# Kernel optimization log

Measured on AMD Instinct MI355X. Metric: run time of the kernel, lower is better.

Reference implementation:

```python
import jax, jax.numpy as jnp
import numpy as np
from jax import lax

IN_H, IN_W = 328, 512
ANCHOR_W, ANCHOR_H = 0.2, 0.29
CONF_T, IOU_T, K_DET = 0.2, 0.3, 10
EPS = 1e-5


def setup_inputs() -> dict:
    key = jax.random.key(0)
    ks = jax.random.split(key, 20)
    f = jnp.float32
    d = {}
    d['features'] = jax.random.normal(ks[0], (16, 512, 4, 21, 32), f)
    d['conv1_w'] = jax.random.normal(ks[1], (256, 512, 3, 3, 3), f) * np.float32(np.sqrt(2.0 / (512 * 27)))
    d['conv1_b'] = jnp.zeros((256,), f)
    d['bn1_g'] = 1.0 + 0.1 * jax.random.normal(ks[2], (256,), f)
    d['bn1_b'] = 0.1 * jax.random.normal(ks[3], (256,), f)
    d['bn1_m'] = 0.1 * jax.random.normal(ks[4], (256,), f)
    d['bn1_v'] = 0.5 + jax.random.uniform(ks[5], (256,), f)
    d['conv2_w'] = jax.random.normal(ks[6], (128, 256, 3, 3, 3), f) * np.float32(np.sqrt(2.0 / (256 * 27)))
    d['conv2_b'] = jnp.zeros((128,), f)
    d['bn2_g'] = 1.0 + 0.1 * jax.random.normal(ks[7], (128,), f)
    d['bn2_b'] = 0.1 * jax.random.normal(ks[8], (128,), f)
    d['bn2_m'] = 0.1 * jax.random.normal(ks[9], (128,), f)
    d['bn2_v'] = 0.5 + jax.random.uniform(ks[10], (128,), f)
    d['conv3_w'] = jax.random.normal(ks[11], (8, 128, 1, 1, 1), f) * np.float32(np.sqrt(2.0 / 128))
    d['conv3_b'] = jnp.zeros((8,), f)
    d['cls_w'] = 0.01 * jax.random.normal(ks[12], (2, 512), f)
    d['cls_b'] = jnp.zeros((2,), f)
    d['sev_w'] = 0.01 * jax.random.normal(ks[13], (4, 512), f)
    d['sev_b'] = jnp.zeros((4,), f)
    return d


def conv3d(x, w, b, pad):
    y = lax.conv_general_dilated(x, w, (1, 1, 1), [(pad, pad)] * 3,
                                 dimension_numbers=('NCDHW', 'OIDHW', 'NCDHW'))
    return y + b[None, :, None, None, None]


def bn3d(x, g, b, m, v):
    inv = g * lax.rsqrt(v + EPS)
    return x * inv[None, :, None, None, None] + (b - m * inv)[None, :, None, None, None]


def _iou_one_vs_all(box, boxes):
    x1 = jnp.maximum(box[0], boxes[:, 0]); y1 = jnp.maximum(box[1], boxes[:, 1])
    x2 = jnp.minimum(box[2], boxes[:, 2]); y2 = jnp.minimum(box[3], boxes[:, 3])
    inter = jnp.clip(x2 - x1, 0.0) * jnp.clip(y2 - y1, 0.0)
    a1 = (box[2] - box[0]) * (box[3] - box[1])
    a2 = (boxes[:, 2] - boxes[:, 0]) * (boxes[:, 3] - boxes[:, 1])
    return inter / jnp.maximum(a1 + a2 - inter, 1e-9)


def _nms_single(boxes, scores, classes):
    # boxes [N,4], scores [N], classes [N] -> top K_DET greedy NMS picks (fixed shape)
    N = boxes.shape[0]
    sc0 = jnp.where(scores > CONF_T, scores, -1.0)
    idxs = jnp.arange(N)

    def step(sc, _):
        i = jnp.argmax(sc)
        s = sc[i]
        valid = s > 0.0
        box = boxes[i]
        iou = _iou_one_vs_all(box, boxes)
        suppress = (iou > IOU_T) | (idxs == i)
        sc = jnp.where(suppress, -1.0, sc)
        vf = valid.astype(boxes.dtype)
        return sc, (box * vf, jnp.maximum(s, 0.0) * vf, jnp.where(valid, classes[i], -1))

    _, (kb, ks, kc) = lax.scan(step, sc0, None, length=K_DET)
    return kb, ks, kc  # [K,4], [K], [K]


def _decode_and_nms(raw):
    # raw: [B, H, W, 8]
    B, H, W, _ = raw.shape
    xo = jax.nn.sigmoid(raw[..., 0])
    yo = jax.nn.sigmoid(raw[..., 1])
    ws = jnp.exp(raw[..., 2])
    hs = jnp.exp(raw[..., 3])
    obj = jax.nn.sigmoid(raw[..., 4])
    cls_prob = jax.nn.softmax(raw[..., 5:], axis=-1)
    gx = (jnp.arange(W, dtype=raw.dtype) / W)[None, None, :]
    gy = (jnp.arange(H, dtype=raw.dtype) / H)[None, :, None]
    xc = (gx + xo) * IN_W
    yc = (gy + yo) * IN_H
    bw = ANCHOR_W * ws * IN_W
    bh = ANCHOR_H * hs * IN_H
    boxes = jnp.stack([xc - bw / 2, yc - bh / 2, xc + bw / 2, yc + bh / 2], axis=-1)
    best_score = jnp.max(cls_prob, axis=-1)
    best_idx = jnp.argmax(cls_prob, axis=-1).astype(jnp.int32)
    conf = obj * best_score
    N = H * W
    boxes = boxes.reshape(B, N, 4)
    conf = conf.reshape(B, N)
    best_idx = best_idx.reshape(B, N)
    return jax.vmap(_nms_single)(boxes, conf, best_idx)


def reference(features, conv1_w, conv1_b, bn1_g, bn1_b, bn1_m, bn1_v,
              conv2_w, conv2_b, bn2_g, bn2_b, bn2_m, bn2_v,
              conv3_w, conv3_b, cls_w, cls_b, sev_w, sev_b):
    # classification heads (global avg pool; dropout = identity in eval)
    pooled = features.mean(axis=(2, 3, 4))  # [B, 512]
    clip_pred = pooled @ cls_w.T + cls_b
    severity_pred = pooled @ sev_w.T + sev_b
    # detection head
    x = jax.nn.relu(bn3d(conv3d(features, conv1_w, conv1_b, 1), bn1_g, bn1_b, bn1_m, bn1_v))
    x = jax.nn.relu(bn3d(conv3d(x, conv2_w, conv2_b, 1), bn2_g, bn2_b, bn2_m, bn2_v))
    raw = conv3d(x, conv3_w, conv3_b, 0)          # [B, 8, T, H, W]
    raw = raw.mean(axis=2)                        # [B, 8, H, W]  (mean over time)
    raw = jnp.transpose(raw, (0, 2, 3, 1))        # [B, H, W, 8]  (A=1)
    det_boxes, det_scores, det_classes = _decode_and_nms(raw)
    return clip_pred, severity_pred, det_boxes, det_scores, det_classes
```

## Files before the change

### kernel.cpp

```cpp
#include <hip/hip_runtime.h>

typedef _Float16 f16;
typedef _Float16 f16x8 __attribute__((ext_vector_type(8)));
typedef float f32x4 __attribute__((ext_vector_type(4)));

#define DHW 2688
#define HW_ 672

__device__ __forceinline__ void gload16(const void* g, void* l) {
    __builtin_amdgcn_global_load_lds((const __attribute__((address_space(1))) void*)g,
                                     (__attribute__((address_space(3))) void*)l, 16, 0, 0);
}

__global__ __launch_bounds__(256) void init_k(f16* a, f16* b, f16* c, f16* d)
{
    int t = threadIdx.x;
    a[2 * t] = (f16)0.f; a[2 * t + 1] = (f16)0.f;
    b[2 * t] = (f16)0.f; b[2 * t + 1] = (f16)0.f;
    c[2 * t] = (f16)0.f; c[2 * t + 1] = (f16)0.f;
    d[2 * t] = (f16)0.f; d[2 * t + 1] = (f16)0.f;
}

__global__ __launch_bounds__(256) void wsplit_k(
    const float* __restrict__ w, const float* __restrict__ convb,
    const float* __restrict__ bng, const float* __restrict__ bnb,
    const float* __restrict__ bnm, const float* __restrict__ bnv,
    f16* __restrict__ wh, f16* __restrict__ wl, float* __restrict__ shift,
    int CO, int CI)
{
    int idx = blockIdx.x * 256 + threadIdx.x;
    int total = CO * CI * 27;
    if (idx >= total) return;
    int ci = idx % CI; int t = idx / CI; int co = t % CO; int o = t / CO;
    float scale = bng[co] / sqrtf(bnv[co] + 1e-5f);
    float x = w[((long)co * CI + ci) * 27 + o] * scale;
    f16 h = (f16)x;
    wh[idx] = h;
    wl[idx] = (f16)(x - (float)h);
    if (o == 0 && ci == 0) shift[co] = (convb[co] - bnm[co]) * scale + bnb[co];
}

__global__ __launch_bounds__(256) void fsplit_k(const float* __restrict__ X,
                                                f16* __restrict__ Fh, f16* __restrict__ Fl)
{
    __shared__ float s[64][65];
    const int t = threadIdx.x;
    const int dhw0 = blockIdx.x * 64, ci0 = blockIdx.y * 64, b = blockIdx.z;
    const int d = t & 63, c0 = t >> 6;
#pragma unroll
    for (int p = 0; p < 16; ++p) {
        int c = p * 4 + c0;
        s[c][d] = X[((long)(b * 512 + ci0 + c)) * DHW + dhw0 + d];
    }
    __syncthreads();
#pragma unroll
    for (int p = 0; p < 2; ++p) {
        int dd = (t >> 3) + p * 32, g = t & 7;
        f16x8 hv, lv;
#pragma unroll
        for (int j = 0; j < 8; ++j) {
            float v = s[g * 8 + j][dd];
            f16 h = (f16)v;
            hv[j] = h;
            lv[j] = (f16)(v - (float)h);
        }
        long oidx = ((long)b * DHW + dhw0 + dd) * 512 + ci0 + g * 8;
        *(f16x8*)&Fh[oidx] = hv;
        *(f16x8*)&Fl[oidx] = lv;
    }
}

template<int CO, int CI, int BM, int BN, int TH, int WM, int WN, int OUTS>
__global__ __launch_bounds__(TH, (TH == 512) ? 4 : 3) void convk(
    const f16* __restrict__ Xh, const f16* __restrict__ Xl,
    const f16* __restrict__ Whi, const f16* __restrict__ Wlo,
    const float* __restrict__ shift, long ZOFF,
    f16* __restrict__ Yh, f16* __restrict__ Yl, float* __restrict__ Yf)
{
    static_assert(BN == 128, "grid.x mapping assumes BN==128");
    constexpr int AIT = BM * 8 / TH;
    constexpr int BIT = BN * 8 / TH;
    constexpr int MI = (BM / WM) / 16;
    constexpr int NI = (BN / WN) / 16;

    __shared__ __align__(16) char sm[(BM + BN) * 256];
    f16* Ah = (f16*)sm;
    f16* Al = Ah + BM * 64;
    f16* Bh = Al + BM * 64;
    f16* Bl = Bh + BN * 64;
    __shared__ float s_shift[BM];

    const int tid = threadIdx.x, lane = tid & 63, wid = tid >> 6;
    const int wm = wid / WN, wn = wid % WN;
    const int wmbase = wm * (BM / WM), wnbase = wn * (BN / WN);
    const int kg = lane >> 4;
    const int nb = blockIdx.x;
    const int bimg = nb / 21;
    const int dhw0 = (nb % 21) * BN;
    const int cobase = blockIdx.y * BM;

    if (tid < BM) s_shift[tid] = shift[cobase + tid];

    int a_co[AIT], a_cig8[AIT], a_ldsg[AIT];
#pragma unroll
    for (int it = 0; it < AIT; ++it) {
        int g = it * TH + tid;
        a_co[it] = g >> 3;
        a_cig8[it] = ((g & 7) ^ (a_co[it] & 7)) << 3;
        a_ldsg[it] = (it * TH + (tid & ~63)) * 8;
    }
    int b_cig8[BIT], b_ldsg[BIT], b_dd[BIT], b_hh[BIT], b_ww[BIT];
#pragma unroll
    for (int it = 0; it < BIT; ++it) {
        int g = it * TH + tid;
        int n = g >> 3;
        b_cig8[it] = ((g & 7) ^ (n & 7)) << 3;
        b_ldsg[it] = (it * TH + (tid & ~63)) * 8;
        int ng = dhw0 + n;
        b_dd[it] = ng / HW_;
        int r = ng % HW_;
        b_hh[it] = r >> 5;
        b_ww[it] = r & 31;
    }

    f32x4 acc[MI][NI];
    f32x4 zero = {0.f, 0.f, 0.f, 0.f};
#pragma unroll
    for (int i = 0; i < MI; ++i)
#pragma unroll
        for (int j = 0; j < NI; ++j) acc[i][j] = zero;

    for (int o = 0; o < 27; ++o) {
        const int od = o / 9 - 1, ohh = (o / 3) % 3 - 1, oww = o % 3 - 1;
        int aoff[AIT];
        long boff[BIT];
#pragma unroll
        for (int it = 0; it < AIT; ++it)
            aoff[it] = (o * CO + cobase + a_co[it]) * CI + a_cig8[it];
#pragma unroll
        for (int it = 0; it < BIT; ++it) {
            int d2 = b_dd[it] + od, h2 = b_hh[it] + ohh, w2 = b_ww[it] + oww;
            bool val = ((unsigned)d2 < 4u) & ((unsigned)h2 < 21u) & ((unsigned)w2 < 32u);
            boff[it] = val ? ((long)(bimg * DHW + d2 * HW_ + h2 * 32 + w2) * CI + b_cig8[it])
                           : ZOFF;
        }
        for (int ci0 = 0; ci0 < CI; ci0 += 64) {
            __syncthreads();
#pragma unroll
            for (int it = 0; it < AIT; ++it) {
                gload16(Whi + aoff[it] + ci0, Ah + a_ldsg[it]);
                gload16(Wlo + aoff[it] + ci0, Al + a_ldsg[it]);
            }
#pragma unroll
            for (int it = 0; it < BIT; ++it) {
                gload16(Xh + boff[it] + ci0, Bh + b_ldsg[it]);
                gload16(Xl + boff[it] + ci0, Bl + b_ldsg[it]);
            }
            __syncthreads();
#pragma unroll
            for (int ks = 0; ks < 2; ++ks) {
                f16x8 ah[MI], al[MI], bh[NI], bl[NI];
#pragma unroll
                for (int mi = 0; mi < MI; ++mi) {
                    int row = wmbase + mi * 16 + (lane & 15);
                    int pos = (((ks << 2) | kg) ^ (row & 7)) << 3;
                    ah[mi] = *(const f16x8*)&Ah[row * 64 + pos];
                    al[mi] = *(const f16x8*)&Al[row * 64 + pos];
                }
#pragma unroll
                for (int ni = 0; ni < NI; ++ni) {
                    int row = wnbase + ni * 16 + (lane & 15);
                    int pos = (((ks << 2) | kg) ^ (row & 7)) << 3;
                    bh[ni] = *(const f16x8*)&Bh[row * 64 + pos];
                    bl[ni] = *(const f16x8*)&Bl[row * 64 + pos];
                }
#pragma unroll
                for (int mi = 0; mi < MI; ++mi)
#pragma unroll
                    for (int ni = 0; ni < NI; ++ni) {
                        acc[mi][ni] = __builtin_amdgcn_mfma_f32_16x16x32_f16(ah[mi], bh[ni], acc[mi][ni], 0, 0, 0);
                        acc[mi][ni] = __builtin_amdgcn_mfma_f32_16x16x32_f16(ah[mi], bl[ni], acc[mi][ni], 0, 0, 0);
                        acc[mi][ni] = __builtin_amdgcn_mfma_f32_16x16x32_f16(al[mi], bh[ni], acc[mi][ni], 0, 0, 0);
                    }
            }
        }
    }

    const long nrow0 = (long)bimg * DHW + dhw0;
    __syncthreads();
    if (OUTS) {
        f16* T = (f16*)sm;
#pragma unroll
        for (int part = 0; part < 2; ++part) {
#pragma unroll
            for (int mi = 0; mi < MI; ++mi)
#pragma unroll
                for (int ni = 0; ni < NI; ++ni) {
                    int n_l = wnbase + ni * 16 + (lane & 15);
                    int co_l = wmbase + mi * 16 + ((lane >> 4) << 2);
#pragma unroll
                    for (int r = 0; r < 4; ++r) {
                        float v = acc[mi][ni][r] + s_shift[co_l + r];
                        v = fmaxf(v, 0.f);
                        f16 h = (f16)v;
                        T[n_l * BM + co_l + r] = part ? (f16)(v - (float)h) : h;
                    }
                }
            __syncthreads();
            f16* Yp = part ? Yl : Yh;
#pragma unroll
            for (int wg = 0; wg < BN * BM / 8 / TH; ++wg) {
                int g = wg * TH + tid;
                int n = g / (BM / 8), gg = g % (BM / 8);
                *(f16x8*)(Yp + (nrow0 + n) * CO + cobase + gg * 8) = *(const f16x8*)&T[n * BM + gg * 8];
            }
            __syncthreads();
        }
    } else {
        float* T = (float*)sm;
#pragma unroll
        for (int mi = 0; mi < MI; ++mi)
#pragma unroll
            for (int ni = 0; ni < NI; ++ni) {
                int n_l = wnbase + ni * 16 + (lane & 15);
                int co_l = wmbase + mi * 16 + ((lane >> 4) << 2);
#pragma unroll
                for (int r = 0; r < 4; ++r) {
                    float v = acc[mi][ni][r] + s_shift[co_l + r];
                    T[n_l * BM + co_l + r] = fmaxf(v, 0.f);
                }
            }
        __syncthreads();
#pragma unroll
        for (int wg = 0; wg < BN * BM / 4 / TH; ++wg) {
            int g = wg * TH + tid;
            int n = g / (BM / 4), gg = g % (BM / 4);
            *(float4*)(Yf + (nrow0 + n) * CO + cobase + gg * 4) = *(const float4*)&T[n * BM + gg * 4];
        }
    }
}

__global__ __launch_bounds__(256) void pool_k(const float* __restrict__ F, float* __restrict__ pooled)
{
    int b = blockIdx.x, cblk = blockIdx.y;
    int tid = threadIdx.x, lane = tid & 63, wid = tid >> 6;
    const float* Fb = F + ((long)b * 512 + cblk * 32) * DHW;
    for (int c = wid; c < 32; c += 4) {
        const float* row = Fb + (long)c * DHW;
        float s = 0.f;
        for (int i = lane; i < DHW; i += 64) s += row[i];
#pragma unroll
        for (int o2 = 32; o2; o2 >>= 1) s += __shfl_down(s, o2);
        if (lane == 0) pooled[b * 512 + cblk * 32 + c] = s / 2688.f;
    }
}

__global__ __launch_bounds__(128) void head2_k(const float* __restrict__ pooled,
    const float* __restrict__ cw, const float* __restrict__ cb,
    const float* __restrict__ sw, const float* __restrict__ sb,
    float* __restrict__ out)
{
    int t = threadIdx.x;
    if (t >= 96) return;
    int b = t & 15, o = t >> 4;
    const float* p = pooled + b * 512;
    const float* wr = (o < 2) ? (cw + o * 512) : (sw + (o - 2) * 512);
    float s = 0.f;
    for (int i = 0; i < 512; ++i) s += p[i] * wr[i];
    if (o < 2) out[b * 2 + o] = s + cb[o];
    else out[32 + b * 4 + (o - 2)] = s + sb[o - 2];
}

__global__ __launch_bounds__(256) void dec_k(const float* __restrict__ X2,
    const float* __restrict__ w3, const float* __restrict__ b3,
    float* __restrict__ boxes, float* __restrict__ conf, float* __restrict__ cls)
{
    __shared__ float swt[1024];
    int tid = threadIdx.x;
    for (int i = tid; i < 1024; i += 256) swt[i] = w3[i];
    __syncthreads();
    int idx = blockIdx.x * 256 + tid;
    int b = idx / HW_, hw = idx % HW_;
    int h = hw >> 5, w = hw & 31;
    float a[8];
#pragma unroll
    for (int c = 0; c < 8; ++c) a[c] = 0.f;
#pragma unroll
    for (int t4 = 0; t4 < 4; ++t4) {
        const float4* xp = (const float4*)(X2 + ((long)b * DHW + t4 * HW_ + hw) * 128);
#pragma unroll 8
        for (int cg = 0; cg < 32; ++cg) {
            float4 x = xp[cg];
#pragma unroll
            for (int c = 0; c < 8; ++c) {
                a[c] = fmaf(swt[c * 128 + cg * 4 + 0], x.x, a[c]);
                a[c] = fmaf(swt[c * 128 + cg * 4 + 1], x.y, a[c]);
                a[c] = fmaf(swt[c * 128 + cg * 4 + 2], x.z, a[c]);
                a[c] = fmaf(swt[c * 128 + cg * 4 + 3], x.w, a[c]);
            }
        }
    }
    float raw[8];
#pragma unroll
    for (int c = 0; c < 8; ++c) raw[c] = a[c] * 0.25f + b3[c];
    float xo = 1.f / (1.f + expf(-raw[0]));
    float yo = 1.f / (1.f + expf(-raw[1]));
    float wsc = expf(raw[2]);
    float hsc = expf(raw[3]);
    float obj = 1.f / (1.f + expf(-raw[4]));
    float mx = fmaxf(raw[5], fmaxf(raw[6], raw[7]));
    float e0 = expf(raw[5] - mx), e1 = expf(raw[6] - mx), e2 = expf(raw[7] - mx);
    float se = e0 + e1 + e2;
    int bi = 0; float bs = e0;
    if (e1 > bs) { bi = 1; bs = e1; }
    if (e2 > bs) { bi = 2; bs = e2; }
    float best = bs / se;
    float gx = (float)w * (1.f / 32.f);
    float gy = (float)h / 21.f;
    float xc = (gx + xo) * 512.f;
    float yc = (gy + yo) * 328.f;
    float bw = 0.2f * wsc * 512.f;
    float bh = 0.29f * hsc * 328.f;
    long bo = (long)idx * 4;
    boxes[bo + 0] = xc - bw * 0.5f;
    boxes[bo + 1] = yc - bh * 0.5f;
    boxes[bo + 2] = xc + bw * 0.5f;
    boxes[bo + 3] = yc + bh * 0.5f;
    conf[idx] = obj * best;
    cls[idx] = (float)bi;
}

__global__ __launch_bounds__(256) void nms_k(const float* __restrict__ boxes,
    const float* __restrict__ conf, const float* __restrict__ cls,
    float* __restrict__ out)
{
    int b = blockIdx.x, tid = threadIdx.x;
    int lane = tid & 63, wid = tid >> 6;
    __shared__ float sc[HW_];
    __shared__ float4 sb[HW_];
    __shared__ float sk[HW_];
    __shared__ float rv[4];
    __shared__ int ri[4];
    const float* cf = conf + b * HW_;
    const float4* bx = (const float4*)(boxes + (long)b * HW_ * 4);
    for (int i = tid; i < HW_; i += 256) {
        float c = cf[i];
        sc[i] = (c > 0.2f) ? c : -1.f;
        sb[i] = bx[i];
        sk[i] = cls[b * HW_ + i];
    }
    __syncthreads();
    for (int it = 0; it < 10; ++it) {
        float bv = -2.f; int bidx = 1 << 20;
        for (int i = tid; i < HW_; i += 256) {
            float v = sc[i];
            if (v > bv || (v == bv && i < bidx)) { bv = v; bidx = i; }
        }
#pragma unroll
        for (int o2 = 32; o2; o2 >>= 1) {
            float ov = __shfl_down(bv, o2);
            int oi = __shfl_down(bidx, o2);
            if (ov > bv || (ov == bv && oi < bidx)) { bv = ov; bidx = oi; }
        }
        if (lane == 0) { rv[wid] = bv; ri[wid] = bidx; }
        __syncthreads();
        if (tid == 0) {
#pragma unroll
            for (int wv = 1; wv < 4; ++wv)
                if (rv[wv] > rv[0] || (rv[wv] == rv[0] && ri[wv] < ri[0])) { rv[0] = rv[wv]; ri[0] = ri[wv]; }
        }
        __syncthreads();
        float s = rv[0]; int ix = ri[0];
        float4 wb = sb[ix];
        bool valid = s > 0.f;
        for (int i = tid; i < HW_; i += 256) {
            float4 ob = sb[i];
            float x1 = fmaxf(wb.x, ob.x), y1 = fmaxf(wb.y, ob.y);
            float x2 = fminf(wb.z, ob.z), y2 = fminf(wb.w, ob.w);
            float inter = fmaxf(x2 - x1, 0.f) * fmaxf(y2 - y1, 0.f);
            float a1 = (wb.z - wb.x) * (wb.w - wb.y);
            float a2 = (ob.z - ob.x) * (ob.w - ob.y);
            float iou = inter / fmaxf(a1 + a2 - inter, 1e-9f);
            if (iou > 0.3f || i == ix) sc[i] = -1.f;
        }
        if (tid == 0) {
            float vf = valid ? 1.f : 0.f;
            float* ob2 = out + 96 + (b * 10 + it) * 4;
            ob2[0] = wb.x * vf; ob2[1] = wb.y * vf; ob2[2] = wb.z * vf; ob2[3] = wb.w * vf;
            out[736 + b * 10 + it] = valid ? s : 0.f;
            out[896 + b * 10 + it] = valid ? sk[ix] : -1.f;
        }
        __syncthreads();
    }
}

extern "C" void kernel_launch(void* const* d_in, const int* in_sizes, int n_in,
                              void* d_out, int out_size, void* d_ws, size_t ws_size,
                              hipStream_t stream)
{
    const float* features = (const float*)d_in[0];
    const float* c1w = (const float*)d_in[1];
    const float* c1b = (const float*)d_in[2];
    const float* g1 = (const float*)d_in[3];
    const float* b1 = (const float*)d_in[4];
    const float* m1 = (const float*)d_in[5];
    const float* v1 = (const float*)d_in[6];
    const float* c2w = (const float*)d_in[7];
    const float* c2b = (const float*)d_in[8];
    const float* g2 = (const float*)d_in[9];
    const float* b2 = (const float*)d_in[10];
    const float* m2 = (const float*)d_in[11];
    const float* v2 = (const float*)d_in[12];
    const float* c3w = (const float*)d_in[13];
    const float* c3b = (const float*)d_in[14];
    const float* clw = (const float*)d_in[15];
    const float* clb = (const float*)d_in[16];
    const float* svw = (const float*)d_in[17];
    const float* svb = (const float*)d_in[18];
    float* out = (float*)d_out;

    char* wsp = (char*)d_ws;
    size_t off = 0;
    auto alloc = [&](size_t bytes) -> char* {
        char* p = wsp + off;
        off += (bytes + 255) & ~(size_t)255;
        return p;
    };
    const long NPIX = 16L * DHW;
    const long ZF = NPIX * 512;
    const long ZA = NPIX * 256;

    f16* w1h = (f16*)alloc(27ULL * 256 * 512 * 2);
    f16* w1l = (f16*)alloc(27ULL * 256 * 512 * 2);
    f16* w2h = (f16*)alloc(27ULL * 128 * 256 * 2);
    f16* w2l = (f16*)alloc(27ULL * 128 * 256 * 2);
    float* sh1 = (float*)alloc(256 * 4);
    float* sh2 = (float*)alloc(128 * 4);
    f16* Fh = (f16*)alloc(ZF * 2 + 1024);
    f16* Fl = (f16*)alloc(ZF * 2 + 1024);
    f16* a1h = (f16*)alloc(ZA * 2 + 1024);
    f16* a1l = (f16*)alloc(ZA * 2 + 1024);
    float* act2 = (float*)alloc((size_t)NPIX * 128 * 4);
    float* pooled = (float*)alloc(16 * 512 * 4);
    float* bxs = (float*)alloc(16ULL * HW_ * 4 * 4);
    float* cnf = (float*)alloc(16 * HW_ * 4);
    float* clsv = (float*)alloc(16 * HW_ * 4);

    hipLaunchKernelGGL(init_k, dim3(1), dim3(256), 0, stream, Fh + ZF, Fl + ZF, a1h + ZA, a1l + ZA);
    hipLaunchKernelGGL(wsplit_k, dim3((256 * 512 * 27 + 255) / 256), dim3(256), 0, stream,
                       c1w, c1b, g1, b1, m1, v1, w1h, w1l, sh1, 256, 512);
    hipLaunchKernelGGL(wsplit_k, dim3((128 * 256 * 27 + 255) / 256), dim3(256), 0, stream,
                       c2w, c2b, g2, b2, m2, v2, w2h, w2l, sh2, 128, 256);
    hipLaunchKernelGGL(fsplit_k, dim3(42, 8, 16), dim3(256), 0, stream, features, Fh, Fl);
    hipLaunchKernelGGL(pool_k, dim3(16, 16), dim3(256), 0, stream, features, pooled);
    hipLaunchKernelGGL(head2_k, dim3(1), dim3(128), 0, stream, pooled, clw, clb, svw, svb, out);
    hipLaunchKernelGGL((convk<256, 512, 128, 128, 512, 2, 4, 1>), dim3(336, 2), dim3(512), 0, stream,
                       Fh, Fl, w1h, w1l, sh1, ZF, a1h, a1l, (float*)nullptr);
    hipLaunchKernelGGL((convk<128, 256, 64, 128, 256, 1, 4, 0>), dim3(336, 2), dim3(256), 0, stream,
                       a1h, a1l, w2h, w2l, sh2, ZA, (f16*)nullptr, (f16*)nullptr, act2);
    hipLaunchKernelGGL(dec_k, dim3(42), dim3(256), 0, stream, act2, c3w, c3b, bxs, cnf, clsv);
    hipLaunchKernelGGL(nms_k, dim3(16), dim3(256), 0, stream, bxs, cnf, clsv, out);
}
```

Measured before the change: 1.402 ms.

## Double-buffer conv K-loop with async LDS loads and flatten to 32-channel steps

Replaces the single-buffer load/sync/compute loop in the implicit-GEMM conv kernel with a two-stage LDS pipeline: the next 32-channel chunk is issued via global_load_lds while the current one feeds MFMAs, gated by vmcnt waits and raw barriers, with raised wave priority during MFMA. The K loop is flattened over (tap, chunk) and each thread loads exactly one granule per array, with a new swizzle. The second conv now uses 128x128 tiles with 512 threads and a single grid row instead of 64x128 with 256 threads. This aims to hide global load latency behind compute, at the cost of halved per-step K depth (more barriers) and fewer blocks for conv2.

```diff
diff --git a/kernel.cpp b/kernel.cpp
--- a/kernel.cpp
+++ b/kernel.cpp
@@ -6,6 +6,8 @@
 
 #define DHW 2688
 #define HW_ 672
+
+#define WAITVM(N) asm volatile("s_waitcnt vmcnt(" #N ")" ::: "memory")
 
 __device__ __forceinline__ void gload16(const void* g, void* l) {
     __builtin_amdgcn_global_load_lds((const __attribute__((address_space(1))) void*)g,
@@ -71,24 +73,21 @@
 }
 
 template<int CO, int CI, int BM, int BN, int TH, int WM, int WN, int OUTS>
-__global__ __launch_bounds__(TH, (TH == 512) ? 4 : 3) void convk(
+__global__ __launch_bounds__(TH, 4) void convk(
     const f16* __restrict__ Xh, const f16* __restrict__ Xl,
     const f16* __restrict__ Whi, const f16* __restrict__ Wlo,
     const float* __restrict__ shift, long ZOFF,
     f16* __restrict__ Yh, f16* __restrict__ Yl, float* __restrict__ Yf)
 {
-    static_assert(BN == 128, "grid.x mapping assumes BN==128");
-    constexpr int AIT = BM * 8 / TH;
-    constexpr int BIT = BN * 8 / TH;
+    static_assert(BN == 128 && BM == 128 && TH == 512, "one granule per thread per array");
+    constexpr int NC = CI / 32;
+    constexpr int LNC = (NC == 16) ? 4 : 3;
+    constexpr int T_ = 27 * NC;
     constexpr int MI = (BM / WM) / 16;
     constexpr int NI = (BN / WN) / 16;
-
-    __shared__ __align__(16) char sm[(BM + BN) * 256];
-    f16* Ah = (f16*)sm;
-    f16* Al = Ah + BM * 64;
-    f16* Bh = Al + BM * 64;
-    f16* Bl = Bh + BN * 64;
-    __shared__ float s_shift[BM];
+    constexpr int BUFB = (BM + BN) * 128;
+
+    __shared__ __align__(16) char sm[2][BUFB];
 
     const int tid = threadIdx.x, lane = tid & 63, wid = tid >> 6;
     const int wm = wid / WN, wn = wid % WN;
@@ -99,28 +98,41 @@
     const int dhw0 = (nb % 21) * BN;
     const int cobase = blockIdx.y * BM;
 
-    if (tid < BM) s_shift[tid] = shift[cobase + tid];
-
-    int a_co[AIT], a_cig8[AIT], a_ldsg[AIT];
-#pragma unroll
-    for (int it = 0; it < AIT; ++it) {
-        int g = it * TH + tid;
-        a_co[it] = g >> 3;
-        a_cig8[it] = ((g & 7) ^ (a_co[it] & 7)) << 3;
-        a_ldsg[it] = (it * TH + (tid & ~63)) * 8;
-    }
-    int b_cig8[BIT], b_ldsg[BIT], b_dd[BIT], b_hh[BIT], b_ww[BIT];
-#pragma unroll
-    for (int it = 0; it < BIT; ++it) {
-        int g = it * TH + tid;
-        int n = g >> 3;
-        b_cig8[it] = ((g & 7) ^ (n & 7)) << 3;
-        b_ldsg[it] = (it * TH + (tid & ~63)) * 8;
-        int ng = dhw0 + n;
-        b_dd[it] = ng / HW_;
-        int r = ng % HW_;
-        b_hh[it] = r >> 5;
-        b_ww[it] = r & 31;
+    const int srow = tid >> 2;
+    const int ciswz = ((tid & 3) ^ ((tid >> 3) & 3)) << 3;
+    const int ngl = dhw0 + srow;
+    const int dd = ngl / HW_;
+    const int hh = (ngl % HW_) >> 5;
+    const int ww = ngl & 31;
+    const long arowCI = (long)(cobase + srow) * CI + ciswz;
+    const long bpix0 = (long)bimg * DHW;
+    char* const dst0 = &sm[0][0] + ((tid & ~63) << 4);
+    char* const dst1 = &sm[1][0] + ((tid & ~63) << 4);
+
+    auto stage = [&](int ti, char* dst) {
+        int o = ti >> LNC;
+        int c32 = (ti & (NC - 1)) << 5;
+        int od = o / 9; int r9 = o - od * 9; int oh = r9 / 3; int ow = r9 - oh * 3;
+        int d2 = dd + od - 1, h2 = hh + oh - 1, w2 = ww + ow - 1;
+        bool val = ((unsigned)d2 < 4u) & ((unsigned)h2 < 21u) & ((unsigned)w2 < 32u);
+        long asrc = (long)o * (CO * CI) + arowCI + c32;
+        long bsrc = val ? ((bpix0 + d2 * HW_ + h2 * 32 + w2) * CI + ciswz + c32) : ZOFF;
+        gload16(Whi + asrc, dst);
+        gload16(Wlo + asrc, dst + BM * 64);
+        gload16(Xh + bsrc, dst + BM * 128);
+        gload16(Xl + bsrc, dst + BM * 128 + BN * 64);
+    };
+
+    int aidx[MI], bidx[NI];
+#pragma unroll
+    for (int mi = 0; mi < MI; ++mi) {
+        int row = wmbase + mi * 16 + (lane & 15);
+        aidx[mi] = row * 32 + ((kg ^ ((row >> 1) & 3)) << 3);
+    }
+#pragma unroll
+    for (int ni = 0; ni < NI; ++ni) {
+        int row = wnbase + ni * 16 + (lane & 15);
+        bidx[ni] = row * 32 + ((kg ^ ((row >> 1) & 3)) << 3);
     }
 
     f32x4 acc[MI][NI];
@@ -130,66 +142,54 @@
 #pragma unroll
         for (int j = 0; j < NI; ++j) acc[i][j] = zero;
 
-    for (int o = 0; o < 27; ++o) {
-        const int od = o / 9 - 1, ohh = (o / 3) % 3 - 1, oww = o % 3 - 1;
-        int aoff[AIT];
-        long boff[BIT];
-#pragma unroll
-        for (int it = 0; it < AIT; ++it)
-            aoff[it] = (o * CO + cobase + a_co[it]) * CI + a_cig8[it];
-#pragma unroll
-        for (int it = 0; it < BIT; ++it) {
-            int d2 = b_dd[it] + od, h2 = b_hh[it] + ohh, w2 = b_ww[it] + oww;
-            bool val = ((unsigned)d2 < 4u) & ((unsigned)h2 < 21u) & ((unsigned)w2 < 32u);
-            boff[it] = val ? ((long)(bimg * DHW + d2 * HW_ + h2 * 32 + w2) * CI + b_cig8[it])
-                           : ZOFF;
-        }
-        for (int ci0 = 0; ci0 < CI; ci0 += 64) {
-            __syncthreads();
-#pragma unroll
-            for (int it = 0; it < AIT; ++it) {
-                gload16(Whi + aoff[it] + ci0, Ah + a_ldsg[it]);
-                gload16(Wlo + aoff[it] + ci0, Al + a_ldsg[it]);
+    auto compute = [&](const char* buf) {
+        const f16* Ah = (const f16*)buf;
+        const f16* Al = (const f16*)(buf + BM * 64);
+        const f16* Bh = (const f16*)(buf + BM * 128);
+        const f16* Bl = (const f16*)(buf + BM * 128 + BN * 64);
+        f16x8 ah[MI], al[MI], bh[NI], bl[NI];
+#pragma unroll
+        for (int mi = 0; mi < MI; ++mi) {
+            ah[mi] = *(const f16x8*)&Ah[aidx[mi]];
+            al[mi] = *(const f16x8*)&Al[aidx[mi]];
+        }
+#pragma unroll
+        for (int ni = 0; ni < NI; ++ni) {
+            bh[ni] = *(const f16x8*)&Bh[bidx[ni]];
+            bl[ni] = *(const f16x8*)&Bl[bidx[ni]];
+        }
+        __builtin_amdgcn_s_setprio(1);
+#pragma unroll
+        for (int mi = 0; mi < MI; ++mi)
+#pragma unroll
+            for (int ni = 0; ni < NI; ++ni) {
+                acc[mi][ni] = __builtin_amdgcn_mfma_f32_16x16x32_f16(ah[mi], bh[ni], acc[mi][ni], 0, 0, 0);
+                acc[mi][ni] = __builtin_amdgcn_mfma_f32_16x16x32_f16(ah[mi], bl[ni], acc[mi][ni], 0, 0, 0);
+                acc[mi][ni] = __builtin_amdgcn_mfma_f32_16x16x32_f16(al[mi], bh[ni], acc[mi][ni], 0, 0, 0);
             }
-#pragma unroll
-            for (int it = 0; it < BIT; ++it) {
-                gload16(Xh + boff[it] + ci0, Bh + b_ldsg[it]);
-                gload16(Xl + boff[it] + ci0, Bl + b_ldsg[it]);
-            }
-            __syncthreads();
-#pragma unroll
-            for (int ks = 0; ks < 2; ++ks) {
-                f16x8 ah[MI], al[MI], bh[NI], bl[NI];
-#pragma unroll
-                for (int mi = 0; mi < MI; ++mi) {
-                    int row = wmbase + mi * 16 + (lane & 15);
-                    int pos = (((ks << 2) | kg) ^ (row & 7)) << 3;
-                    ah[mi] = *(const f16x8*)&Ah[row * 64 + pos];
-                    al[mi] = *(const f16x8*)&Al[row * 64 + pos];
-                }
-#pragma unroll
-                for (int ni = 0; ni < NI; ++ni) {
-                    int row = wnbase + ni * 16 + (lane & 15);
-                    int pos = (((ks << 2) | kg) ^ (row & 7)) << 3;
-                    bh[ni] = *(const f16x8*)&Bh[row * 64 + pos];
-                    bl[ni] = *(const f16x8*)&Bl[row * 64 + pos];
-                }
-#pragma unroll
-                for (int mi = 0; mi < MI; ++mi)
-#pragma unroll
-                    for (int ni = 0; ni < NI; ++ni) {
-                        acc[mi][ni] = __builtin_amdgcn_mfma_f32_16x16x32_f16(ah[mi], bh[ni], acc[mi][ni], 0, 0, 0);
-                        acc[mi][ni] = __builtin_amdgcn_mfma_f32_16x16x32_f16(ah[mi], bl[ni], acc[mi][ni], 0, 0, 0);
-                        acc[mi][ni] = __builtin_amdgcn_mfma_f32_16x16x32_f16(al[mi], bh[ni], acc[mi][ni], 0, 0, 0);
-                    }
-            }
-        }
-    }
+        __builtin_amdgcn_s_setprio(0);
+    };
+
+    stage(0, dst0);
+    for (int t = 0; t < T_ - 1; ++t) {
+        const int cur = t & 1;
+        stage(t + 1, cur ? dst0 : dst1);
+        WAITVM(4);
+        __builtin_amdgcn_s_barrier();
+        __builtin_amdgcn_sched_barrier(0);
+        compute(&sm[cur][0]);
+        __builtin_amdgcn_sched_barrier(0);
+        __builtin_amdgcn_s_barrier();
+    }
+    WAITVM(0);
+    __builtin_amdgcn_s_barrier();
+    __builtin_amdgcn_sched_barrier(0);
+    compute(&sm[(T_ - 1) & 1][0]);
 
     const long nrow0 = (long)bimg * DHW + dhw0;
     __syncthreads();
     if (OUTS) {
-        f16* T = (f16*)sm;
+        f16* T = (f16*)&sm[0][0];
 #pragma unroll
         for (int part = 0; part < 2; ++part) {
 #pragma unroll
@@ -200,7 +200,7 @@
                     int co_l = wmbase + mi * 16 + ((lane >> 4) << 2);
 #pragma unroll
                     for (int r = 0; r < 4; ++r) {
-                        float v = acc[mi][ni][r] + s_shift[co_l + r];
+                        float v = acc[mi][ni][r] + shift[cobase + co_l + r];
                         v = fmaxf(v, 0.f);
                         f16 h = (f16)v;
                         T[n_l * BM + co_l + r] = part ? (f16)(v - (float)h) : h;
@@ -217,7 +217,7 @@
             __syncthreads();
         }
     } else {
-        float* T = (float*)sm;
+        float* T = (float*)&sm[0][0];
 #pragma unroll
         for (int mi = 0; mi < MI; ++mi)
 #pragma unroll
@@ -226,7 +226,7 @@
                 int co_l = wmbase + mi * 16 + ((lane >> 4) << 2);
 #pragma unroll
                 for (int r = 0; r < 4; ++r) {
-                    float v = acc[mi][ni][r] + s_shift[co_l + r];
+                    float v = acc[mi][ni][r] + shift[cobase + co_l + r];
                     T[n_l * BM + co_l + r] = fmaxf(v, 0.f);
                 }
             }
@@ -456,7 +456,7 @@
     hipLaunchKernelGGL(head2_k, dim3(1), dim3(128), 0, stream, pooled, clw, clb, svw, svb, out);
     hipLaunchKernelGGL((convk<256, 512, 128, 128, 512, 2, 4, 1>), dim3(336, 2), dim3(512), 0, stream,
                        Fh, Fl, w1h, w1l, sh1, ZF, a1h, a1l, (float*)nullptr);
-    hipLaunchKernelGGL((convk<128, 256, 64, 128, 256, 1, 4, 0>), dim3(336, 2), dim3(256), 0, stream,
+    hipLaunchKernelGGL((convk<128, 256, 128, 128, 512, 2, 4, 0>), dim3(336, 1), dim3(512), 0, stream,
                        a1h, a1l, w2h, w2l, sh2, ZA, (f16*)nullptr, (f16*)nullptr, act2);
     hipLaunchKernelGGL(dec_k, dim3(42), dim3(256), 0, stream, act2, c3w, c3b, bxs, cnf, clsv);
     hipLaunchKernelGGL(nms_k, dim3(16), dim3(256), 0, stream, bxs, cnf, clsv, out);
```

New measurement: 1.566 ms. 11.8% more time.

## Switch conv GEMM to 32x32x16 MFMA with fixed 128x128 tiles

Applied to the files above, without the earlier changes.

The implicit-GEMM conv kernel now uses 32x32x16 f16 MFMA instructions instead of 16x16x32. Each wave computes a 64x32 tile with two 16-wide accumulator vectors, and the LDS fragment indices are precomputed outside the main loop. The second conv now uses the same 128x128, 512-thread geometry, so its grid has half as many blocks. The shared shift buffer is dropped in favour of direct global reads in the epilogue. The larger MFMA is meant to cut LDS fragment traffic and instruction count per flop, at the cost of fewer blocks for conv2.

```diff
diff --git a/kernel.cpp b/kernel.cpp
--- a/kernel.cpp
+++ b/kernel.cpp
@@ -2,7 +2,7 @@
 
 typedef _Float16 f16;
 typedef _Float16 f16x8 __attribute__((ext_vector_type(8)));
-typedef float f32x4 __attribute__((ext_vector_type(4)));
+typedef float f32x16 __attribute__((ext_vector_type(16)));
 
 #define DHW 2688
 #define HW_ 672
@@ -70,36 +70,31 @@
     }
 }
 
-template<int CO, int CI, int BM, int BN, int TH, int WM, int WN, int OUTS>
-__global__ __launch_bounds__(TH, (TH == 512) ? 4 : 3) void convk(
+template<int CO, int CI, int BM, int BN, int TH, int OUTS>
+__global__ __launch_bounds__(TH, 4) void convk(
     const f16* __restrict__ Xh, const f16* __restrict__ Xl,
     const f16* __restrict__ Whi, const f16* __restrict__ Wlo,
     const float* __restrict__ shift, long ZOFF,
     f16* __restrict__ Yh, f16* __restrict__ Yl, float* __restrict__ Yf)
 {
-    static_assert(BN == 128, "grid.x mapping assumes BN==128");
-    constexpr int AIT = BM * 8 / TH;
-    constexpr int BIT = BN * 8 / TH;
-    constexpr int MI = (BM / WM) / 16;
-    constexpr int NI = (BN / WN) / 16;
+    static_assert(BN == 128 && BM == 128 && TH == 512, "fixed geometry");
+    constexpr int AIT = 2;
+    constexpr int BIT = 2;
+    constexpr int MI = 2;
 
     __shared__ __align__(16) char sm[(BM + BN) * 256];
     f16* Ah = (f16*)sm;
     f16* Al = Ah + BM * 64;
     f16* Bh = Al + BM * 64;
     f16* Bl = Bh + BN * 64;
-    __shared__ float s_shift[BM];
 
     const int tid = threadIdx.x, lane = tid & 63, wid = tid >> 6;
-    const int wm = wid / WN, wn = wid % WN;
-    const int wmbase = wm * (BM / WM), wnbase = wn * (BN / WN);
-    const int kg = lane >> 4;
+    const int wm = wid >> 2, wn = wid & 3;
+    const int wmbase = wm * 64, wnbase = wn * 32;
     const int nb = blockIdx.x;
     const int bimg = nb / 21;
     const int dhw0 = (nb % 21) * BN;
     const int cobase = blockIdx.y * BM;
-
-    if (tid < BM) s_shift[tid] = shift[cobase + tid];
 
     int a_co[AIT], a_cig8[AIT], a_ldsg[AIT];
 #pragma unroll
@@ -123,12 +118,24 @@
         b_ww[it] = r & 31;
     }
 
-    f32x4 acc[MI][NI];
-    f32x4 zero = {0.f, 0.f, 0.f, 0.f};
+    int aidx[4][MI], bidx[4];
+#pragma unroll
+    for (int ks = 0; ks < 4; ++ks) {
+        int lg = (ks << 1) | (lane >> 5);
+#pragma unroll
+        for (int mi = 0; mi < MI; ++mi) {
+            int row = wmbase + mi * 32 + (lane & 31);
+            aidx[ks][mi] = row * 64 + ((lg ^ (row & 7)) << 3);
+        }
+        int rb = wnbase + (lane & 31);
+        bidx[ks] = rb * 64 + ((lg ^ (rb & 7)) << 3);
+    }
+
+    f32x16 acc[MI];
 #pragma unroll
     for (int i = 0; i < MI; ++i)
 #pragma unroll
-        for (int j = 0; j < NI; ++j) acc[i][j] = zero;
+        for (int r = 0; r < 16; ++r) acc[i][r] = 0.f;
 
     for (int o = 0; o < 27; ++o) {
         const int od = o / 9 - 1, ohh = (o / 3) % 3 - 1, oww = o % 3 - 1;
@@ -141,7 +148,7 @@
         for (int it = 0; it < BIT; ++it) {
             int d2 = b_dd[it] + od, h2 = b_hh[it] + ohh, w2 = b_ww[it] + oww;
             bool val = ((unsigned)d2 < 4u) & ((unsigned)h2 < 21u) & ((unsigned)w2 < 32u);
-            boff[it] = val ? ((long)(bimg * DHW + d2 * HW_ + h2 * 32 + w2) * CI + b_cig8[it])
+            boff[it] = val ? ((long)((bimg * DHW) + d2 * HW_ + h2 * 32 + w2) * CI + b_cig8[it])
                            : ZOFF;
         }
         for (int ci0 = 0; ci0 < CI; ci0 += 64) {
@@ -158,35 +165,25 @@
             }
             __syncthreads();
 #pragma unroll
-            for (int ks = 0; ks < 2; ++ks) {
-                f16x8 ah[MI], al[MI], bh[NI], bl[NI];
-#pragma unroll
-                for (int mi = 0; mi < MI; ++mi) {
-                    int row = wmbase + mi * 16 + (lane & 15);
-                    int pos = (((ks << 2) | kg) ^ (row & 7)) << 3;
-                    ah[mi] = *(const f16x8*)&Ah[row * 64 + pos];
-                    al[mi] = *(const f16x8*)&Al[row * 64 + pos];
-                }
-#pragma unroll
-                for (int ni = 0; ni < NI; ++ni) {
-                    int row = wnbase + ni * 16 + (lane & 15);
-                    int pos = (((ks << 2) | kg) ^ (row & 7)) << 3;
-                    bh[ni] = *(const f16x8*)&Bh[row * 64 + pos];
-                    bl[ni] = *(const f16x8*)&Bl[row * 64 + pos];
-                }
-#pragma unroll
-                for (int mi = 0; mi < MI; ++mi)
-#pragma unroll
-                    for (int ni = 0; ni < NI; ++ni) {
-                        acc[mi][ni] = __builtin_amdgcn_mfma_f32_16x16x32_f16(ah[mi], bh[ni], acc[mi][ni], 0, 0, 0);
-                        acc[mi][ni] = __builtin_amdgcn_mfma_f32_16x16x32_f16(ah[mi], bl[ni], acc[mi][ni], 0, 0, 0);
-                        acc[mi][ni] = __builtin_amdgcn_mfma_f32_16x16x32_f16(al[mi], bh[ni], acc[mi][ni], 0, 0, 0);
-                    }
+            for (int ks = 0; ks < 4; ++ks) {
+                f16x8 ah0 = *(const f16x8*)&Ah[aidx[ks][0]];
+                f16x8 ah1 = *(const f16x8*)&Ah[aidx[ks][1]];
+                f16x8 al0 = *(const f16x8*)&Al[aidx[ks][0]];
+                f16x8 al1 = *(const f16x8*)&Al[aidx[ks][1]];
+                f16x8 bhv = *(const f16x8*)&Bh[bidx[ks]];
+                f16x8 blv = *(const f16x8*)&Bl[bidx[ks]];
+                acc[0] = __builtin_amdgcn_mfma_f32_32x32x16_f16(ah0, bhv, acc[0], 0, 0, 0);
+                acc[0] = __builtin_amdgcn_mfma_f32_32x32x16_f16(ah0, blv, acc[0], 0, 0, 0);
+                acc[0] = __builtin_amdgcn_mfma_f32_32x32x16_f16(al0, bhv, acc[0], 0, 0, 0);
+                acc[1] = __builtin_amdgcn_mfma_f32_32x32x16_f16(ah1, bhv, acc[1], 0, 0, 0);
+                acc[1] = __builtin_amdgcn_mfma_f32_32x32x16_f16(ah1, blv, acc[1], 0, 0, 0);
+                acc[1] = __builtin_amdgcn_mfma_f32_32x32x16_f16(al1, bhv, acc[1], 0, 0, 0);
             }
         }
     }
 
     const long nrow0 = (long)bimg * DHW + dhw0;
+    const int n_l = wnbase + (lane & 31);
     __syncthreads();
     if (OUTS) {
         f16* T = (f16*)sm;
@@ -195,16 +192,12 @@
 #pragma unroll
             for (int mi = 0; mi < MI; ++mi)
 #pragma unroll
-                for (int ni = 0; ni < NI; ++ni) {
-                    int n_l = wnbase + ni * 16 + (lane & 15);
-                    int co_l = wmbase + mi * 16 + ((lane >> 4) << 2);
-#pragma unroll
-                    for (int r = 0; r < 4; ++r) {
-                        float v = acc[mi][ni][r] + s_shift[co_l + r];
-                        v = fmaxf(v, 0.f);
-                        f16 h = (f16)v;
-                        T[n_l * BM + co_l + r] = part ? (f16)(v - (float)h) : h;
-                    }
+                for (int r = 0; r < 16; ++r) {
+                    int co_l = wmbase + mi * 32 + (r & 3) + ((r >> 2) << 3) + ((lane >> 5) << 2);
+                    float v = acc[mi][r] + shift[cobase + co_l];
+                    v = fmaxf(v, 0.f);
+                    f16 h = (f16)v;
+                    T[n_l * BM + co_l] = part ? (f16)(v - (float)h) : h;
                 }
             __syncthreads();
             f16* Yp = part ? Yl : Yh;
@@ -221,14 +214,10 @@
 #pragma unroll
         for (int mi = 0; mi < MI; ++mi)
 #pragma unroll
-            for (int ni = 0; ni < NI; ++ni) {
-                int n_l = wnbase + ni * 16 + (lane & 15);
-                int co_l = wmbase + mi * 16 + ((lane >> 4) << 2);
-#pragma unroll
-                for (int r = 0; r < 4; ++r) {
-                    float v = acc[mi][ni][r] + s_shift[co_l + r];
-                    T[n_l * BM + co_l + r] = fmaxf(v, 0.f);
-                }
+            for (int r = 0; r < 16; ++r) {
+                int co_l = wmbase + mi * 32 + (r & 3) + ((r >> 2) << 3) + ((lane >> 5) << 2);
+                float v = acc[mi][r] + shift[cobase + co_l];
+                T[n_l * BM + co_l] = fmaxf(v, 0.f);
             }
         __syncthreads();
 #pragma unroll
@@ -454,9 +443,9 @@
     hipLaunchKernelGGL(fsplit_k, dim3(42, 8, 16), dim3(256), 0, stream, features, Fh, Fl);
     hipLaunchKernelGGL(pool_k, dim3(16, 16), dim3(256), 0, stream, features, pooled);
     hipLaunchKernelGGL(head2_k, dim3(1), dim3(128), 0, stream, pooled, clw, clb, svw, svb, out);
-    hipLaunchKernelGGL((convk<256, 512, 128, 128, 512, 2, 4, 1>), dim3(336, 2), dim3(512), 0, stream,
+    hipLaunchKernelGGL((convk<256, 512, 128, 128, 512, 1>), dim3(336, 2), dim3(512), 0, stream,
                        Fh, Fl, w1h, w1l, sh1, ZF, a1h, a1l, (float*)nullptr);
-    hipLaunchKernelGGL((convk<128, 256, 64, 128, 256, 1, 4, 0>), dim3(336, 2), dim3(256), 0, stream,
+    hipLaunchKernelGGL((convk<128, 256, 128, 128, 512, 0>), dim3(336, 1), dim3(512), 0, stream,
                        a1h, a1l, w2h, w2l, sh2, ZA, (f16*)nullptr, (f16*)nullptr, act2);
     hipLaunchKernelGGL(dec_k, dim3(42), dim3(256), 0, stream, act2, c3w, c3b, bxs, cnf, clsv);
     hipLaunchKernelGGL(nms_k, dim3(16), dim3(256), 0, stream, bxs, cnf, clsv, out);
```

Measured after the change: 1.543 ms. 10.1% more time.
